# Optimization experiments

Hardware: AMD Instinct MI355X
Metric: run time of the kernel (lower is better)

Reference implementation:

```python
import jax, jax.numpy as jnp
import numpy as np

N = 50000      # nodes
K = 12         # neighbors per node (regular graph, required by e.view(-1, numNgbrs))
E = N * K      # edges, sorted by row
F_IN = 128
F_OUT = 128
ALPHA = 0.2    # LeakyReLU negative slope


def setup_inputs() -> dict:
    key = jax.random.key(0)
    k_x, k_col, k_ws, k_wn, k_a, k_b = jax.random.split(key, 6)
    x = jax.random.normal(k_x, (N, F_IN), dtype=jnp.float32)
    # edges sorted by destination row, exactly K per node
    row = jnp.repeat(jnp.arange(N, dtype=jnp.int32), K)
    col = jax.random.randint(k_col, (E,), 0, N, dtype=jnp.int32)
    adj_vals = jnp.ones((E,), dtype=jnp.float32)  # sparse adj values
    stdv = 1.0 / np.sqrt(F_OUT)
    W_self = jax.random.uniform(k_ws, (F_IN, F_OUT), jnp.float32, -stdv, stdv)
    W_neighbor = jax.random.uniform(k_wn, (F_IN, F_OUT), jnp.float32, -stdv, stdv)
    lim = 1.414 * np.sqrt(6.0 / (2 * F_OUT + 1))  # xavier_uniform gain=1.414 on [2F,1]
    a = jax.random.uniform(k_a, (2 * F_OUT,), jnp.float32, -lim, lim)
    bias = jax.random.uniform(k_b, (F_OUT,), jnp.float32, -stdv, stdv)
    return {"x": x, "adj_vals": adj_vals, "row": row, "col": col,
            "W_self": W_self, "W_neighbor": W_neighbor, "a": a, "bias": bias}


def reference(x, adj_vals, row, col, W_self, W_neighbor, a, bias):
    act_self = x @ W_self                       # [N, F_OUT]
    h = x @ W_neighbor                          # [N, F_OUT]
    # cat([h_in, h_out], 1) @ a  ==  h_in @ a[:F] + h_out @ a[F:]
    # precompute per-node dots, then gather per edge (cheaper than ExF gathers)
    s_in = h @ a[:F_OUT]                        # [N]
    s_out = h @ a[F_OUT:]                       # [N]
    e = jax.nn.leaky_relu(s_in[row] + s_out[col], ALPHA)   # [E]
    # per-destination-node softmax over its K contiguous edges
    att = jax.nn.softmax(e.reshape(N, K), axis=1).reshape(-1)  # [E]
    # attention-weighted sparse scatter-add aggregation
    msg = (adj_vals * att)[:, None] * h[col]    # [E, F_OUT]
    act_neighbor = jax.ops.segment_sum(msg, row, num_segments=N)
    return act_self + act_neighbor + bias
```

## Files before the change

kernel.cpp:

```cpp
#include <hip/hip_runtime.h>

constexpr int N_NODES = 50000;
constexpr int KNB = 12;
constexpr int F = 128;
constexpr float ALPHA = 0.2f;
constexpr int BM = 64;

typedef __bf16 bf16x8 __attribute__((ext_vector_type(8)));
typedef float  f32x4  __attribute__((ext_vector_type(4)));

__device__ __forceinline__ unsigned bfr(float f) {
    unsigned u = __float_as_uint(f);
    return (u + 0x7fffu + ((u >> 16) & 1u)) >> 16;
}
__device__ __forceinline__ unsigned pack2(float lo, float hi) {
    return bfr(lo) | (bfr(hi) << 16);
}
__device__ __forceinline__ float bf2f(unsigned bits16) {
    return __uint_as_float(bits16 << 16);
}

__global__ __launch_bounds__(256) void gat_prep(const float* __restrict__ Wself,
                                                const float* __restrict__ Wnb,
                                                unsigned* __restrict__ Wt) {
    const int gid = blockIdx.x * 256 + threadIdx.x;
    const int n  = gid >> 6;
    const int kp = gid & 63;
    const float* src = (n < F) ? (Wself + n) : (Wnb + (n - F));
    const float f0 = src[(size_t)(kp * 2)     * F];
    const float f1 = src[(size_t)(kp * 2 + 1) * F];
    Wt[n * 64 + kp] = pack2(f0, f1);
}

__global__ __launch_bounds__(256, 2) void gat_gemm(
    const float* __restrict__ x,
    const unsigned* __restrict__ Wt,
    const float* __restrict__ a,
    const float* __restrict__ bias,
    float* __restrict__ out,
    unsigned short* __restrict__ hb,
    float* __restrict__ s_in,
    float* __restrict__ s_out)
{
    __shared__ uint4 ldsX[BM * 16];
    __shared__ uint4 ldsW[256 * 16];

    const int t = threadIdx.x;
    const int base = blockIdx.x * BM;

    const uint4* Wt4 = reinterpret_cast<const uint4*>(Wt);
#pragma unroll
    for (int i = 0; i < 16; ++i) {
        const int idx = t + i * 256;
        const int n   = idx >> 4;
        const int k16 = idx & 15;
        ldsW[n * 16 + (k16 ^ (n & 7))] = Wt4[idx];
    }
#pragma unroll
    for (int i = 0; i < 4; ++i) {
        const int idx = t + i * 256;
        const int row = idx >> 4;
        const int k16 = idx & 15;
        int gr = base + row; if (gr >= N_NODES) gr = N_NODES - 1;
        const float4* xp = reinterpret_cast<const float4*>(x + (size_t)gr * F + k16 * 8);
        const float4 f0 = xp[0];
        const float4 f1 = xp[1];
        uint4 v;
        v.x = pack2(f0.x, f0.y); v.y = pack2(f0.z, f0.w);
        v.z = pack2(f1.x, f1.y); v.w = pack2(f1.z, f1.w);
        ldsX[row * 16 + (k16 ^ (row & 7))] = v;
    }
    __syncthreads();

    const int w    = t >> 6;
    const int lane = t & 63;
    const int lq   = lane >> 4;
    const int lr   = lane & 15;

    const bf16x8* fx = reinterpret_cast<const bf16x8*>(ldsX);
    const bf16x8* fw = reinterpret_cast<const bf16x8*>(ldsW);

    f32x4 acc[4][4];
#pragma unroll
    for (int mt = 0; mt < 4; ++mt)
#pragma unroll
        for (int rt = 0; rt < 4; ++rt)
            acc[mt][rt] = f32x4{0.f, 0.f, 0.f, 0.f};

#pragma unroll
    for (int s = 0; s < 4; ++s) {
        bf16x8 wf[4], xf[4];
#pragma unroll
        for (int mt = 0; mt < 4; ++mt) {
            const int n = w * 64 + mt * 16 + lr;
            wf[mt] = fw[n * 16 + ((s * 4 + lq) ^ (n & 7))];
        }
#pragma unroll
        for (int rt = 0; rt < 4; ++rt) {
            const int r = rt * 16 + lr;
            xf[rt] = fx[r * 16 + ((s * 4 + lq) ^ (r & 7))];
        }
#pragma unroll
        for (int mt = 0; mt < 4; ++mt)
#pragma unroll
            for (int rt = 0; rt < 4; ++rt)
                acc[mt][rt] = __builtin_amdgcn_mfma_f32_16x16x32_bf16(wf[mt], xf[rt], acc[mt][rt], 0, 0, 0);
    }

    __syncthreads();
    float* sbuf = reinterpret_cast<float*>(ldsX);

    if (w < 2) {
#pragma unroll
        for (int mt = 0; mt < 4; ++mt) {
            const int col0 = w * 64 + mt * 16 + lq * 4;
            const float4 b4 = *reinterpret_cast<const float4*>(bias + col0);
#pragma unroll
            for (int rt = 0; rt < 4; ++rt) {
                const int row = base + rt * 16 + lr;
                if (row < N_NODES) {
                    const f32x4 v = acc[mt][rt];
                    float4 o{v[0] + b4.x, v[1] + b4.y, v[2] + b4.z, v[3] + b4.w};
                    *reinterpret_cast<float4*>(out + (size_t)row * F + col0) = o;
                }
            }
        }
    } else {
        float spin[4] = {0.f, 0.f, 0.f, 0.f};
        float spout[4] = {0.f, 0.f, 0.f, 0.f};
#pragma unroll
        for (int mt = 0; mt < 4; ++mt) {
            const int colh0 = (w - 2) * 64 + mt * 16 + lq * 4;
            const float4 al = *reinterpret_cast<const float4*>(a + colh0);
            const float4 ah = *reinterpret_cast<const float4*>(a + F + colh0);
#pragma unroll
            for (int rt = 0; rt < 4; ++rt) {
                const int row = base + rt * 16 + lr;
                const f32x4 v = acc[mt][rt];
                if (row < N_NODES) {
                    uint2 pk{pack2(v[0], v[1]), pack2(v[2], v[3])};
                    *reinterpret_cast<uint2*>(hb + (size_t)row * F + colh0) = pk;
                }
                spin[rt]  = fmaf(v[0], al.x, fmaf(v[1], al.y, fmaf(v[2], al.z, fmaf(v[3], al.w, spin[rt]))));
                spout[rt] = fmaf(v[0], ah.x, fmaf(v[1], ah.y, fmaf(v[2], ah.z, fmaf(v[3], ah.w, spout[rt]))));
            }
        }
#pragma unroll
        for (int rt = 0; rt < 4; ++rt) {
            spin[rt]  += __shfl_xor(spin[rt], 16);
            spin[rt]  += __shfl_xor(spin[rt], 32);
            spout[rt] += __shfl_xor(spout[rt], 16);
            spout[rt] += __shfl_xor(spout[rt], 32);
        }
        if (lq == 0) {
#pragma unroll
            for (int rt = 0; rt < 4; ++rt) {
                sbuf[(w - 2) * 128 + rt * 16 + lr]      = spin[rt];
                sbuf[(w - 2) * 128 + 64 + rt * 16 + lr] = spout[rt];
            }
        }
    }
    __syncthreads();
    if (t < 128) {
        const int i = t & 63;
        const int row = base + i;
        if (row < N_NODES) {
            if (t < 64) s_in[row]  = sbuf[i] + sbuf[128 + i];
            else        s_out[row] = sbuf[64 + i] + sbuf[192 + i];
        }
    }
}

__global__ __launch_bounds__(256) void gat_attn(
    const uint2* __restrict__ hbU2,
    const float* __restrict__ s_in,
    const float* __restrict__ s_out,
    const int* __restrict__ colidx,
    const float* __restrict__ adj,
    float* __restrict__ out)
{
    const int wid  = threadIdx.x >> 6;
    const int lane = threadIdx.x & 63;
    const int node = blockIdx.x * 4 + wid;
    const int half = lane >> 5;
    const int hl   = lane & 31;

    float e = -1e30f;
    int c = 0;
    float av = 0.f;
    if (lane < KNB) {
        c  = colidx[node * KNB + lane];
        av = adj[node * KNB + lane];
        const float ev = s_in[node] + s_out[c];
        e = ev > 0.f ? ev : ALPHA * ev;
    }
    float m = e;
#pragma unroll
    for (int msk = 8; msk >= 1; msk >>= 1) m = fmaxf(m, __shfl_xor(m, msk));
    const float p = (lane < KNB) ? __expf(e - m) : 0.f;
    float ssum = p;
#pragma unroll
    for (int msk = 8; msk >= 1; msk >>= 1) ssum += __shfl_xor(ssum, msk);
    const float att = p / ssum * av;

    float4 acc{0.f, 0.f, 0.f, 0.f};
    const int sbase = half * 6;
#pragma unroll
    for (int i = 0; i < 6; ++i) {
        const float aj = __shfl(att, sbase + i);
        const int   cj = __shfl(c,   sbase + i);
        const uint2 u = hbU2[(size_t)cj * 32 + hl];
        acc.x = fmaf(aj, bf2f(u.x & 0xffffu), acc.x);
        acc.y = fmaf(aj, bf2f(u.x >> 16),     acc.y);
        acc.z = fmaf(aj, bf2f(u.y & 0xffffu), acc.z);
        acc.w = fmaf(aj, bf2f(u.y >> 16),     acc.w);
    }
    acc.x += __shfl_xor(acc.x, 32);
    acc.y += __shfl_xor(acc.y, 32);
    acc.z += __shfl_xor(acc.z, 32);
    acc.w += __shfl_xor(acc.w, 32);

    if (lane < 32) {
        float4* op = reinterpret_cast<float4*>(out + (size_t)node * F) + hl;
        float4 o = *op;
        o.x += acc.x; o.y += acc.y; o.z += acc.z; o.w += acc.w;
        *op = o;
    }
}

extern "C" void kernel_launch(void* const* d_in, const int* in_sizes, int n_in,
                              void* d_out, int out_size, void* d_ws, size_t ws_size,
                              hipStream_t stream) {
    const float* x     = (const float*)d_in[0];
    const float* adj   = (const float*)d_in[1];
    const int*   col   = (const int*)d_in[3];
    const float* Wself = (const float*)d_in[4];
    const float* Wnb   = (const float*)d_in[5];
    const float* a     = (const float*)d_in[6];
    const float* bias  = (const float*)d_in[7];
    float* out = (float*)d_out;

    char* ws = (char*)d_ws;
    unsigned short* hb = (unsigned short*)ws;
    float* s_in  = (float*)(ws + 12800000);
    float* s_out = (float*)(ws + 13000000);
    unsigned* Wt = (unsigned*)(ws + 13200000);

    gat_prep<<<64, 256, 0, stream>>>(Wself, Wnb, Wt);
    gat_gemm<<<(N_NODES + BM - 1) / BM, 256, 0, stream>>>(x, Wt, a, bias, out, hb, s_in, s_out);
    gat_attn<<<N_NODES / 4, 256, 0, stream>>>((const uint2*)hb, s_in, s_out, col, adj, out);
}
```

Before: 56.58 us.

## Pre-swizzle weights for direct-to-LDS loads and pack four nodes per wave in attention

gat_prep now writes the bf16 weight matrix already in the XOR-swizzled LDS layout, so gat_gemm can copy it with global_load_lds straight into shared memory without a trip through registers. The attention kernel now gives each node 16 lanes instead of a full wave, and each lane gathers 16-byte chunks of neighbor rows over all 12 edges. This removes the cross-half shuffle reduction and idle lanes, and the wider loads should raise memory-level parallelism for the random row gathers. The costs are a longer serial load chain per lane and a dependence on the compiler placing the vmcnt wait for the LDS-direct loads before the barrier.

```diff
diff --git a/kernel.cpp b/kernel.cpp
--- a/kernel.cpp
+++ b/kernel.cpp
@@ -26,10 +26,12 @@
     const int gid = blockIdx.x * 256 + threadIdx.x;
     const int n  = gid >> 6;
     const int kp = gid & 63;
+    const int k16 = kp >> 2;
+    const int sub = kp & 3;
     const float* src = (n < F) ? (Wself + n) : (Wnb + (n - F));
     const float f0 = src[(size_t)(kp * 2)     * F];
     const float f1 = src[(size_t)(kp * 2 + 1) * F];
-    Wt[n * 64 + kp] = pack2(f0, f1);
+    Wt[n * 64 + (k16 ^ (n & 7)) * 4 + sub] = pack2(f0, f1);
 }
 
 __global__ __launch_bounds__(256, 2) void gat_gemm(
@@ -46,15 +48,19 @@
     __shared__ uint4 ldsW[256 * 16];
 
     const int t = threadIdx.x;
+    const int w    = t >> 6;
+    const int lane = t & 63;
     const int base = blockIdx.x * BM;
 
     const uint4* Wt4 = reinterpret_cast<const uint4*>(Wt);
 #pragma unroll
     for (int i = 0; i < 16; ++i) {
-        const int idx = t + i * 256;
-        const int n   = idx >> 4;
-        const int k16 = idx & 15;
-        ldsW[n * 16 + (k16 ^ (n & 7))] = Wt4[idx];
+        const int ch = w * 16 + i;
+        const uint4* gp = Wt4 + ch * 64 + lane;
+        uint4* lp = ldsW + ch * 64;
+        __builtin_amdgcn_global_load_lds(
+            (const __attribute__((address_space(1))) void*)gp,
+            (__attribute__((address_space(3))) void*)lp, 16, 0, 0);
     }
 #pragma unroll
     for (int i = 0; i < 4; ++i) {
@@ -72,8 +78,6 @@
     }
     __syncthreads();
 
-    const int w    = t >> 6;
-    const int lane = t & 63;
     const int lq   = lane >> 4;
     const int lr   = lane & 15;
 
@@ -172,7 +176,7 @@
 }
 
 __global__ __launch_bounds__(256) void gat_attn(
-    const uint2* __restrict__ hbU2,
+    const uint4* __restrict__ hbU4,
     const float* __restrict__ s_in,
     const float* __restrict__ s_out,
     const int* __restrict__ colidx,
@@ -181,51 +185,52 @@
 {
     const int wid  = threadIdx.x >> 6;
     const int lane = threadIdx.x & 63;
-    const int node = blockIdx.x * 4 + wid;
-    const int half = lane >> 5;
-    const int hl   = lane & 31;
+    const int lr   = lane & 15;
+    const int node = (blockIdx.x * 4 + wid) * 4 + (lane >> 4);
 
     float e = -1e30f;
     int c = 0;
     float av = 0.f;
-    if (lane < KNB) {
-        c  = colidx[node * KNB + lane];
-        av = adj[node * KNB + lane];
+    if (lr < KNB) {
+        c  = colidx[node * KNB + lr];
+        av = adj[node * KNB + lr];
         const float ev = s_in[node] + s_out[c];
         e = ev > 0.f ? ev : ALPHA * ev;
     }
     float m = e;
 #pragma unroll
     for (int msk = 8; msk >= 1; msk >>= 1) m = fmaxf(m, __shfl_xor(m, msk));
-    const float p = (lane < KNB) ? __expf(e - m) : 0.f;
+    const float p = (lr < KNB) ? __expf(e - m) : 0.f;
     float ssum = p;
 #pragma unroll
     for (int msk = 8; msk >= 1; msk >>= 1) ssum += __shfl_xor(ssum, msk);
     const float att = p / ssum * av;
 
-    float4 acc{0.f, 0.f, 0.f, 0.f};
-    const int sbase = half * 6;
-#pragma unroll
-    for (int i = 0; i < 6; ++i) {
-        const float aj = __shfl(att, sbase + i);
-        const int   cj = __shfl(c,   sbase + i);
-        const uint2 u = hbU2[(size_t)cj * 32 + hl];
-        acc.x = fmaf(aj, bf2f(u.x & 0xffffu), acc.x);
-        acc.y = fmaf(aj, bf2f(u.x >> 16),     acc.y);
-        acc.z = fmaf(aj, bf2f(u.y & 0xffffu), acc.z);
-        acc.w = fmaf(aj, bf2f(u.y >> 16),     acc.w);
-    }
-    acc.x += __shfl_xor(acc.x, 32);
-    acc.y += __shfl_xor(acc.y, 32);
-    acc.z += __shfl_xor(acc.z, 32);
-    acc.w += __shfl_xor(acc.w, 32);
-
-    if (lane < 32) {
-        float4* op = reinterpret_cast<float4*>(out + (size_t)node * F) + hl;
-        float4 o = *op;
-        o.x += acc.x; o.y += acc.y; o.z += acc.z; o.w += acc.w;
-        *op = o;
-    }
+    float accf[8];
+#pragma unroll
+    for (int k = 0; k < 8; ++k) accf[k] = 0.f;
+    const int gbase = lane & 48;
+#pragma unroll
+    for (int j = 0; j < KNB; ++j) {
+        const float aj = __shfl(att, gbase + j);
+        const int   cj = __shfl(c,   gbase + j);
+        const uint4 u = hbU4[(size_t)cj * 16 + lr];
+        accf[0] = fmaf(aj, bf2f(u.x & 0xffffu), accf[0]);
+        accf[1] = fmaf(aj, bf2f(u.x >> 16),     accf[1]);
+        accf[2] = fmaf(aj, bf2f(u.y & 0xffffu), accf[2]);
+        accf[3] = fmaf(aj, bf2f(u.y >> 16),     accf[3]);
+        accf[4] = fmaf(aj, bf2f(u.z & 0xffffu), accf[4]);
+        accf[5] = fmaf(aj, bf2f(u.z >> 16),     accf[5]);
+        accf[6] = fmaf(aj, bf2f(u.w & 0xffffu), accf[6]);
+        accf[7] = fmaf(aj, bf2f(u.w >> 16),     accf[7]);
+    }
+    float4* op = reinterpret_cast<float4*>(out + (size_t)node * F + lr * 8);
+    float4 o0 = op[0];
+    float4 o1 = op[1];
+    o0.x += accf[0]; o0.y += accf[1]; o0.z += accf[2]; o0.w += accf[3];
+    o1.x += accf[4]; o1.y += accf[5]; o1.z += accf[6]; o1.w += accf[7];
+    op[0] = o0;
+    op[1] = o1;
 }
 
 extern "C" void kernel_launch(void* const* d_in, const int* in_sizes, int n_in,
@@ -248,5 +253,5 @@
 
     gat_prep<<<64, 256, 0, stream>>>(Wself, Wnb, Wt);
     gat_gemm<<<(N_NODES + BM - 1) / BM, 256, 0, stream>>>(x, Wt, a, bias, out, hb, s_in, s_out);
-    gat_attn<<<N_NODES / 4, 256, 0, stream>>>((const uint2*)hb, s_in, s_out, col, adj, out);
-}
+    gat_attn<<<(N_NODES + 15) / 16, 256, 0, stream>>>((const uint4*)hb, s_in, s_out, col, adj, out);
+}
```

After: 57.14 us. Within noise of the previous version (+1.0%).
